# Kernel optimization log

Measured on AMD Instinct MI355X. Metric: run time of the kernel, lower is better.

Reference implementation:

```python
import jax, jax.numpy as jnp
import numpy as np

EPS = 1e-12  # matches torch F.normalize default eps in spectral_norm


def _l2norm(v):
    return v / jnp.maximum(jnp.linalg.norm(v), EPS)


def _spectral_norm(W, u):
    # One power-iteration step (torch spectral_norm training behavior).
    # u, v are treated as constants w.r.t. gradients.
    v = jax.lax.stop_gradient(_l2norm(W.T @ u))
    u2 = jax.lax.stop_gradient(_l2norm(W @ v))
    sigma = jnp.einsum('o,oi,i->', u2, W, v)
    return W / sigma


def setup_inputs() -> dict:
    key = jax.random.key(0)
    ks = jax.random.split(key, 8)
    B, C, N = 8, 512, 2048
    d = C // 8
    return {
        'x':  jax.random.normal(ks[0], (B, C, N), dtype=jnp.float32),
        'Wq': jax.random.normal(ks[1], (d, C), dtype=jnp.float32) * (1.0 / np.sqrt(C)),
        'Wk': jax.random.normal(ks[2], (d, C), dtype=jnp.float32) * (1.0 / np.sqrt(C)),
        'Wv': jax.random.normal(ks[3], (C, C), dtype=jnp.float32) * (1.0 / np.sqrt(C)),
        'uq': jax.random.normal(ks[4], (d,), dtype=jnp.float32),
        'uk': jax.random.normal(ks[5], (d,), dtype=jnp.float32),
        'uv': jax.random.normal(ks[6], (C,), dtype=jnp.float32),
        'gamma': jax.random.normal(ks[7], (1,), dtype=jnp.float32) * 0.1,
    }


def reference(x, Wq, Wk, Wv, uq, uk, uv, gamma):
    # x: [B, C, N]
    f = jnp.einsum('oi,bin->bon', _spectral_norm(Wq, uq), x)  # [B, C/8, N]
    g = jnp.einsum('oi,bin->bon', _spectral_norm(Wk, uk), x)  # [B, C/8, N]
    h = jnp.einsum('oi,bin->bon', _spectral_norm(Wv, uv), x)  # [B, C, N]
    scores = jnp.einsum('bdn,bdm->bnm', f, g)                 # f^T g: [B, N, N]
    beta = jax.nn.softmax(scores, axis=1)                      # softmax over dim=1
    o = gamma[0] * jnp.einsum('bcn,bnm->bcm', h, beta) + x    # [B, C, N]
    return o
```

## Files before the change

### kernel.cpp

```cpp
#include <hip/hip_runtime.h>
#include <hip/hip_bf16.h>
#include <math.h>

#define B_ 8
#define C_ 512
#define N_ 2048
#define D_ 64
#define O_ 640

typedef __bf16 bf16x8 __attribute__((ext_vector_type(8)));
typedef float f32x4 __attribute__((ext_vector_type(4)));
typedef unsigned short ushort8_t __attribute__((ext_vector_type(8)));
typedef unsigned short ushort4_t __attribute__((ext_vector_type(4)));

__device__ __forceinline__ unsigned short f2bf(float f) {
    unsigned int u = __builtin_bit_cast(unsigned int, f);
    u += 0x7fffu + ((u >> 16) & 1u);
    return (unsigned short)(u >> 16);
}

__device__ __forceinline__ unsigned short f2bf_hw(float f) {
    __bf16 h = (__bf16)f;
    return __builtin_bit_cast(unsigned short, h);
}

__device__ __forceinline__ float fastexp(float x) {
    return exp2f(x * 1.44269504088896340736f);
}

union FragU { ushort8_t u; bf16x8 b; };

__device__ __forceinline__ bf16x8 ldfrag(const unsigned short* p) {
    FragU t; t.u = *(const ushort8_t*)p; return t.b;
}

__device__ __forceinline__ void gload_lds16(const unsigned short* g, unsigned short* l) {
    __builtin_amdgcn_global_load_lds((const __attribute__((address_space(1))) void*)g,
                                     (__attribute__((address_space(3))) void*)l,
                                     16, 0, 0);
}

__global__ __launch_bounds__(512) void k_colvec(const float* __restrict__ Wq,
                                                const float* __restrict__ Wk,
                                                const float* __restrict__ Wv,
                                                const float* __restrict__ uq,
                                                const float* __restrict__ uk,
                                                const float* __restrict__ uv,
                                                float* __restrict__ tpart) {
    int which = blockIdx.y, oq = blockIdx.x;
    const float* W; const float* u; int R;
    if (which == 0)      { W = Wq; u = uq; R = 64;  }
    else if (which == 1) { W = Wk; u = uk; R = 64;  }
    else                 { W = Wv; u = uv; R = 512; }
    int chunk = R >> 2;
    int i = threadIdx.x;
    float s = 0.f;
    int o0 = oq * chunk, o1 = o0 + chunk;
    for (int o = o0; o < o1; ++o) s += W[(size_t)o * 512 + i] * u[o];
    tpart[((which << 2) + oq) * 512 + i] = s;
}

__global__ __launch_bounds__(512) void k_trow(const float* __restrict__ tpart,
                                              float* __restrict__ tvec,
                                              float* __restrict__ t2) {
    int which = blockIdx.x, i = threadIdx.x;
    const float* tp = tpart + (which << 2) * 512;
    float s = tp[i] + tp[512 + i] + tp[1024 + i] + tp[1536 + i];
    tvec[which * 512 + i] = s;
    __shared__ float red[512];
    red[i] = s * s; __syncthreads();
    for (int st = 256; st > 0; st >>= 1) { if (i < st) red[i] += red[i + st]; __syncthreads(); }
    if (i == 0) t2[which] = red[0];
}

__global__ __launch_bounds__(256) void k_rowvec(const float* __restrict__ Wq,
                                                const float* __restrict__ Wk,
                                                const float* __restrict__ Wv,
                                                const float* __restrict__ tvec,
                                                float* __restrict__ wpart) {
    int which = blockIdx.y;
    const float* W; int R;
    if (which == 0)      { W = Wq; R = 64;  }
    else if (which == 1) { W = Wk; R = 64;  }
    else                 { W = Wv; R = 512; }
    int tid = threadIdx.x, lane = tid & 63, wv = tid >> 6;
    int row = blockIdx.x * 4 + wv;
    float ps = 0.f;
    if (row < R) {
        const float4* wr_ = (const float4*)(W + (size_t)row * 512);
        const float4* tv = (const float4*)(tvec + which * 512);
        float4 a0 = wr_[lane * 2], a1 = wr_[lane * 2 + 1];
        float4 b0 = tv[lane * 2], b1 = tv[lane * 2 + 1];
        float s = a0.x * b0.x + a0.y * b0.y + a0.z * b0.z + a0.w * b0.w
                + a1.x * b1.x + a1.y * b1.y + a1.z * b1.z + a1.w * b1.w;
        #pragma unroll
        for (int off = 1; off < 64; off <<= 1) s += __shfl_xor(s, off, 64);
        ps = s * s;
    }
    __shared__ float red[4];
    if (lane == 0) red[wv] = ps;
    __syncthreads();
    if (tid == 0) wpart[which * 128 + blockIdx.x] = red[0] + red[1] + red[2] + red[3];
}

__global__ __launch_bounds__(128) void k_scale(const float* __restrict__ wpart,
                                               const float* __restrict__ t2,
                                               float* __restrict__ scales) {
    int which = blockIdx.x, tid = threadIdx.x;
    float s = wpart[which * 128 + tid];
    #pragma unroll
    for (int off = 1; off < 64; off <<= 1) s += __shfl_xor(s, off, 64);
    __shared__ float r2[2];
    if ((tid & 63) == 0) r2[tid >> 6] = s;
    __syncthreads();
    if (tid == 0) scales[which] = sqrtf(t2[which] / fmaxf(r2[0] + r2[1], 1e-24f));
}

__global__ __launch_bounds__(256) void k_wconv(const float* __restrict__ Wq,
                                               const float* __restrict__ Wk,
                                               const float* __restrict__ Wv,
                                               const float* __restrict__ scales,
                                               unsigned short* __restrict__ Wb) {
    int gid = blockIdx.x * 256 + threadIdx.x;
    int e0 = gid * 8;
    int o = e0 >> 9, i = e0 & 511;
    const float* src; float sc;
    if (o < 64)       { src = Wq + (size_t)o * 512;         sc = scales[0]; }
    else if (o < 128) { src = Wk + (size_t)(o - 64) * 512;  sc = scales[1]; }
    else              { src = Wv + (size_t)(o - 128) * 512; sc = scales[2]; }
    float4 v0 = *(const float4*)(src + i), v1 = *(const float4*)(src + i + 4);
    ushort8_t u;
    u[0] = f2bf(v0.x * sc); u[1] = f2bf(v0.y * sc); u[2] = f2bf(v0.z * sc); u[3] = f2bf(v0.w * sc);
    u[4] = f2bf(v1.x * sc); u[5] = f2bf(v1.y * sc); u[6] = f2bf(v1.z * sc); u[7] = f2bf(v1.w * sc);
    *(ushort8_t*)&Wb[(size_t)o * 512 + i] = u;
}

__global__ __launch_bounds__(256) void k_transpose(const float* __restrict__ x,
                                                   unsigned short* __restrict__ xT) {
    __shared__ float tile[64][33];
    int b = blockIdx.z;
    int n0 = blockIdx.x * 32, c0 = blockIdx.y * 64;
    int tx = threadIdx.x, ty = threadIdx.y;
    #pragma unroll
    for (int k = 0; k < 8; ++k) {
        int c = ty + k * 8;
        tile[c][tx] = x[((size_t)b * C_ + c0 + c) * N_ + n0 + tx];
    }
    __syncthreads();
    #pragma unroll
    for (int k = 0; k < 4; ++k) {
        int n = ty + k * 8;
        unsigned int p = (unsigned int)f2bf(tile[tx * 2][n]) |
                         ((unsigned int)f2bf(tile[tx * 2 + 1][n]) << 16);
        *(unsigned int*)&xT[((size_t)b * N_ + n0 + n) * C_ + c0 + tx * 2] = p;
    }
}

__global__ __launch_bounds__(256) void k_proj(const unsigned short* __restrict__ xT,
                                              const unsigned short* __restrict__ Wb,
                                              unsigned short* __restrict__ fT,
                                              unsigned short* __restrict__ gT,
                                              unsigned short* __restrict__ hb) {
    int b = blockIdx.z, n0 = blockIdx.y * 128, o0 = blockIdx.x * 128;
    int tid = threadIdx.x, lane = tid & 63, w = tid >> 6;
    int wr = w >> 1, wc = w & 1;
    __shared__ __align__(16) unsigned short Sh[16384];
    unsigned short* As = Sh;
    unsigned short* Bs = Sh + 8192;
    f32x4 zero = {0.f, 0.f, 0.f, 0.f};
    f32x4 acc[4][4];
    #pragma unroll
    for (int i = 0; i < 4; ++i)
        #pragma unroll
        for (int j = 0; j < 4; ++j) acc[i][j] = zero;
    int r8 = lane >> 3, s = lane & 7;
    int scol = (s ^ r8) * 8;

    for (int kt = 0; kt < 8; ++kt) {
        #pragma unroll
        for (int q = 0; q < 4; ++q) {
            int chunk = w * 4 + q;
            int row = chunk * 8 + r8;
            gload_lds16(xT + ((size_t)b * N_ + n0 + row) * C_ + kt * 64 + scol, &As[chunk * 512]);
            gload_lds16(Wb + (size_t)(o0 + row) * C_ + kt * 64 + scol, &Bs[chunk * 512]);
        }
        __syncthreads();
        int kg = lane >> 4, r16 = lane & 15;
        #pragma unroll
        for (int kk = 0; kk < 2; ++kk) {
            int sw = kk * 4 + kg;
            bf16x8 af[4];
            #pragma unroll
            for (int i = 0; i < 4; ++i) {
                int row = wr * 64 + i * 16 + r16;
                af[i] = ldfrag(&As[row * 64 + (sw ^ (row & 7)) * 8]);
            }
            #pragma unroll
            for (int j = 0; j < 4; ++j) {
                int row = wc * 64 + j * 16 + r16;
                bf16x8 bv = ldfrag(&Bs[row * 64 + (sw ^ (row & 7)) * 8]);
                #pragma unroll
                for (int i = 0; i < 4; ++i)
                    acc[i][j] = __builtin_amdgcn_mfma_f32_16x16x32_bf16(af[i], bv, acc[i][j], 0, 0, 0);
            }
        }
        __syncthreads();
    }

    unsigned short* St = Sh;
    if (o0 == 0) {
        #pragma unroll
        for (int p = 0; p < 2; ++p) {
            if (wc == p) {
                #pragma unroll
                for (int i = 0; i < 4; ++i)
                    #pragma unroll
                    for (int j = 0; j < 4; ++j)
                        #pragma unroll
                        for (int r = 0; r < 4; ++r)
                            St[(wr * 64 + i * 16 + (lane >> 4) * 4 + r) * 72 + j * 16 + (lane & 15)] = f2bf(acc[i][j][r]);
            }
            __syncthreads();
            unsigned short* dst = p == 0 ? fT : gT;
            #pragma unroll
            for (int it = 0; it < 4; ++it) {
                int row = it * 32 + (tid >> 3);
                *(ushort8_t*)&dst[((size_t)b * N_ + n0 + row) * D_ + (tid & 7) * 8] =
                    *(ushort8_t*)&St[row * 72 + (tid & 7) * 8];
            }
            __syncthreads();
        }
    } else {
        int ho0 = o0 - 128;
        #pragma unroll
        for (int p = 0; p < 2; ++p) {
            if (wc == p) {
                #pragma unroll
                for (int i = 0; i < 4; ++i)
                    #pragma unroll
                    for (int j = 0; j < 4; ++j)
                        #pragma unroll
                        for (int r = 0; r < 4; ++r)
                            St[(j * 16 + (lane & 15)) * 136 + wr * 64 + i * 16 + (lane >> 4) * 4 + r] = f2bf(acc[i][j][r]);
            }
            __syncthreads();
            #pragma unroll
            for (int it = 0; it < 4; ++it) {
                int row = it * 16 + (tid >> 4);
                *(ushort8_t*)&hb[((size_t)b * C_ + ho0 + p * 64 + row) * N_ + n0 + (tid & 15) * 8] =
                    *(ushort8_t*)&St[row * 136 + (tid & 15) * 8];
            }
            __syncthreads();
        }
    }
}

__global__ __launch_bounds__(256) void k_stats(const unsigned short* __restrict__ fT,
                                               const unsigned short* __restrict__ gT,
                                               float* __restrict__ colmax,
                                               float* __restrict__ colsinv) {
    int b = blockIdx.y, m0 = blockIdx.x * 16;
    int tid = threadIdx.x, lane = tid & 63, w = tid >> 6;
    int mcol = m0 + (lane & 15);
    const unsigned short* gbase = gT + ((size_t)b * N_ + mcol) * D_ + (lane >> 4) * 8;
    bf16x8 g0 = ldfrag(gbase);
    bf16x8 g1 = ldfrag(gbase + 32);

    float mx = -1e30f, sm = 0.f;
    for (int nt = w * 32; nt < w * 32 + 32; ++nt) {
        const unsigned short* abase = fT + ((size_t)b * N_ + nt * 16 + (lane & 15)) * D_ + (lane >> 4) * 8;
        f32x4 s = {0.f, 0.f, 0.f, 0.f};
        s = __builtin_amdgcn_mfma_f32_16x16x32_bf16(ldfrag(abase), g0, s, 0, 0, 0);
        s = __builtin_amdgcn_mfma_f32_16x16x32_bf16(ldfrag(abase + 32), g1, s, 0, 0, 0);
        float tm = fmaxf(fmaxf(s[0], s[1]), fmaxf(s[2], s[3]));
        float nm = fmaxf(mx, tm);
        float c = fastexp(mx - nm);
        sm = sm * c + fastexp(s[0] - nm) + fastexp(s[1] - nm) + fastexp(s[2] - nm) + fastexp(s[3] - nm);
        mx = nm;
    }
    #pragma unroll
    for (int off = 16; off < 64; off <<= 1) {
        float omx = __shfl_xor(mx, off, 64);
        float osm = __shfl_xor(sm, off, 64);
        float nm = fmaxf(mx, omx);
        sm = sm * fastexp(mx - nm) + osm * fastexp(omx - nm);
        mx = nm;
    }
    __shared__ float lmx[4][16], lsm[4][16];
    if ((lane >> 4) == 0) { lmx[w][lane & 15] = mx; lsm[w][lane & 15] = sm; }
    __syncthreads();
    if (tid < 16) {
        float M = lmx[0][tid], S = lsm[0][tid];
        #pragma unroll
        for (int q = 1; q < 4; ++q) {
            float om = lmx[q][tid], os = lsm[q][tid];
            float nm = fmaxf(M, om);
            S = S * fastexp(M - nm) + os * fastexp(om - nm);
            M = nm;
        }
        colmax[(size_t)b * N_ + m0 + tid] = M;
        colsinv[(size_t)b * N_ + m0 + tid] = 1.0f / S;
    }
}

__global__ __launch_bounds__(512, 4) void k_av(const unsigned short* __restrict__ fT,
                                               const unsigned short* __restrict__ gT,
                                               const unsigned short* __restrict__ hb,
                                               const float* __restrict__ colmax,
                                               const float* __restrict__ colsinv,
                                               const float* __restrict__ x,
                                               const float* __restrict__ gamma,
                                               float* __restrict__ out) {
    __shared__ __align__(16) unsigned short FT[2][4096];
    __shared__ __align__(16) unsigned short HB[16384];
    __shared__ __align__(16) unsigned short BS[2][4096];

    const int NT = N_ / 64;
    int bid = blockIdx.x;
    int xg = bid & 7, sidx = bid >> 3;
    int mi = sidx & 31, gh = sidx >> 5;
    int g = xg + 8 * gh;
    int b = g >> 1, ch = g & 1;
    int m0 = mi * 64, c0 = ch * 256;

    int tid = threadIdx.x, lane = tid & 63, w = tid >> 6;
    int nw = w & 3, mh = w >> 2;
    int l15 = lane & 15, lq = lane >> 4;
    int r8 = lane >> 3, sl = lane & 7;
    int scol = (sl ^ r8) * 8;

    const float LOG2E = 1.44269504088896340736f;
    bf16x8 gf[2][2];
    float off_[2];
    #pragma unroll
    for (int j = 0; j < 2; ++j) {
        int m = m0 + mh * 32 + j * 16 + l15;
        #pragma unroll
        for (int kd = 0; kd < 2; ++kd)
            gf[j][kd] = ldfrag(gT + ((size_t)b * N_ + m) * D_ + kd * 32 + lq * 8);
        off_[j] = log2f(colsinv[(size_t)b * N_ + m]) - colmax[(size_t)b * N_ + m] * LOG2E;
    }

    f32x4 zero = {0.f, 0.f, 0.f, 0.f};
    f32x4 acc[2][4];
    #pragma unroll
    for (int i = 0; i < 2; ++i)
        #pragma unroll
        for (int j = 0; j < 4; ++j) acc[i][j] = zero;

    const unsigned short* fbase = fT + ((size_t)b * N_) * D_;
    const unsigned short* hbase = hb + ((size_t)b * C_ + c0) * N_;

    ushort8_t hreg0, hreg1, hreg2, hreg3;

    auto HLOAD = [&](int kt) {
        const unsigned short* p0 = hbase + (size_t)((w * 4 + 0) * 8 + r8) * N_ + kt * 64 + scol;
        const unsigned short* p1 = hbase + (size_t)((w * 4 + 1) * 8 + r8) * N_ + kt * 64 + scol;
        const unsigned short* p2 = hbase + (size_t)((w * 4 + 2) * 8 + r8) * N_ + kt * 64 + scol;
        const unsigned short* p3 = hbase + (size_t)((w * 4 + 3) * 8 + r8) * N_ + kt * 64 + scol;
        hreg0 = *(const ushort8_t*)p0;
        hreg1 = *(const ushort8_t*)p1;
        hreg2 = *(const ushort8_t*)p2;
        hreg3 = *(const ushort8_t*)p3;
    };
    auto HWRITE = [&]() {
        *(ushort8_t*)&HB[(w * 4 + 0) * 512 + lane * 8] = hreg0;
        *(ushort8_t*)&HB[(w * 4 + 1) * 512 + lane * 8] = hreg1;
        *(ushort8_t*)&HB[(w * 4 + 2) * 512 + lane * 8] = hreg2;
        *(ushort8_t*)&HB[(w * 4 + 3) * 512 + lane * 8] = hreg3;
    };
    auto STAGE_FT = [&](int kt, int p) {
        gload_lds16(fbase + ((size_t)kt * 64 + w * 8 + r8) * D_ + scol, &FT[p][w * 512]);
    };
    auto SPHASE = [&](int p) {
        int arow = nw * 16 + l15;
        bf16x8 af0 = ldfrag(&FT[p][arow * 64 + ((lq ^ (arow & 7)) * 8)]);
        bf16x8 af1 = ldfrag(&FT[p][arow * 64 + (((4 + lq) ^ (arow & 7)) * 8)]);
        #pragma unroll
        for (int j = 0; j < 2; ++j) {
            f32x4 sv = zero;
            sv = __builtin_amdgcn_mfma_f32_16x16x32_bf16(af0, gf[j][0], sv, 0, 0, 0);
            sv = __builtin_amdgcn_mfma_f32_16x16x32_bf16(af1, gf[j][1], sv, 0, 0, 0);
            int mrel = mh * 32 + j * 16 + l15;
            ushort4_t pk;
            #pragma unroll
            for (int r = 0; r < 4; ++r)
                pk[r] = f2bf_hw(exp2f(fmaf(sv[r], LOG2E, off_[j])));
            int nt = nw * 16 + lq * 4;
            *(ushort4_t*)&BS[p][mrel * 64 + (((nt >> 3) ^ (mrel & 7)) * 8) + (nt & 7)] = pk;
        }
    };
    auto PVPHASE = [&](int p) {
        __builtin_amdgcn_s_setprio(1);
        #pragma unroll
        for (int kk = 0; kk < 2; ++kk) {
            int ng = kk * 4 + lq;
            bf16x8 pa[2];
            #pragma unroll
            for (int i = 0; i < 2; ++i) {
                int mr = mh * 32 + i * 16 + l15;
                pa[i] = ldfrag(&BS[p][mr * 64 + ((ng ^ (mr & 7)) * 8)]);
            }
            #pragma unroll
            for (int j = 0; j < 4; ++j) {
                int cr = nw * 64 + j * 16 + l15;
                bf16x8 hv = ldfrag(&HB[cr * 64 + ((ng ^ (cr & 7)) * 8)]);
                #pragma unroll
                for (int i = 0; i < 2; ++i)
                    acc[i][j] = __builtin_amdgcn_mfma_f32_16x16x32_bf16(pa[i], hv, acc[i][j], 0, 0, 0);
            }
        }
        __builtin_amdgcn_s_setprio(0);
    };

    STAGE_FT(0, 0);
    HLOAD(0);
    asm volatile("s_waitcnt vmcnt(0)" ::: "memory");
    __builtin_amdgcn_sched_barrier(0);
    HWRITE();
    asm volatile("s_waitcnt lgkmcnt(0)" ::: "memory");
    __builtin_amdgcn_sched_barrier(0);
    __builtin_amdgcn_s_barrier();
    __builtin_amdgcn_sched_barrier(0);
    SPHASE(0);
    asm volatile("s_waitcnt lgkmcnt(0)" ::: "memory");
    __builtin_amdgcn_sched_barrier(0);
    __builtin_amdgcn_s_barrier();
    __builtin_amdgcn_sched_barrier(0);

    #pragma unroll 1
    for (int kt = 0; kt < NT; ++kt) {
        int p = kt & 1;
        if (kt + 1 < NT) {
            HLOAD(kt + 1);
            STAGE_FT(kt + 1, p ^ 1);
            __builtin_amdgcn_sched_barrier(0);
        }
        PVPHASE(p);
        if (kt + 1 < NT) {
            asm volatile("s_waitcnt vmcnt(0)" ::: "memory");
            __builtin_amdgcn_sched_barrier(0);
            __builtin_amdgcn_s_barrier();
            __builtin_amdgcn_sched_barrier(0);
            HWRITE();
            SPHASE(p ^ 1);
            asm volatile("s_waitcnt lgkmcnt(0)" ::: "memory");
            __builtin_amdgcn_sched_barrier(0);
            __builtin_amdgcn_s_barrier();
            __builtin_amdgcn_sched_barrier(0);
        }
    }

    float gv = gamma[0];
    #pragma unroll
    for (int i = 0; i < 2; ++i) {
        int mabs = m0 + mh * 32 + i * 16 + lq * 4;
        #pragma unroll
        for (int j = 0; j < 4; ++j) {
            int cabs = c0 + nw * 64 + j * 16 + l15;
            size_t base = ((size_t)b * C_ + cabs) * N_ + mabs;
            float4 xv = *(const float4*)(x + base);
            float4 ov;
            ov.x = gv * acc[i][j][0] + xv.x;
            ov.y = gv * acc[i][j][1] + xv.y;
            ov.z = gv * acc[i][j][2] + xv.z;
            ov.w = gv * acc[i][j][3] + xv.w;
            *(float4*)(out + base) = ov;
        }
    }
}

extern "C" void kernel_launch(void* const* d_in, const int* in_sizes, int n_in,
                              void* d_out, int out_size, void* d_ws, size_t ws_size,
                              hipStream_t stream) {
    const float* x     = (const float*)d_in[0];
    const float* Wq    = (const float*)d_in[1];
    const float* Wk    = (const float*)d_in[2];
    const float* Wv    = (const float*)d_in[3];
    const float* uq    = (const float*)d_in[4];
    const float* uk    = (const float*)d_in[5];
    const float* uv    = (const float*)d_in[6];
    const float* gamma = (const float*)d_in[7];
    float* out = (float*)d_out;

    char* wsb = (char*)d_ws;
    float* scales         = (float*)wsb;
    unsigned short* xT    = (unsigned short*)(wsb + 256);
    unsigned short* fT    = xT + (size_t)B_ * N_ * C_;
    unsigned short* gT    = fT + (size_t)B_ * N_ * D_;
    unsigned short* hb    = gT + (size_t)B_ * N_ * D_;
    float* colmax         = (float*)(hb + (size_t)B_ * C_ * N_);
    float* colsinv        = colmax + (size_t)B_ * N_;
    float* tpart          = colsinv + (size_t)B_ * N_;
    float* tvec           = tpart + 3 * 4 * 512;
    float* t2             = tvec + 3 * 512;
    float* wpart          = t2 + 16;
    unsigned short* Wb    = (unsigned short*)(wpart + 3 * 128);

    k_colvec<<<dim3(4, 3), 512, 0, stream>>>(Wq, Wk, Wv, uq, uk, uv, tpart);
    k_trow<<<3, 512, 0, stream>>>(tpart, tvec, t2);
    k_rowvec<<<dim3(128, 3), 256, 0, stream>>>(Wq, Wk, Wv, tvec, wpart);
    k_scale<<<3, 128, 0, stream>>>(wpart, t2, scales);
    k_wconv<<<O_ * C_ / (256 * 8), 256, 0, stream>>>(Wq, Wk, Wv, scales, Wb);
    k_transpose<<<dim3(N_ / 32, C_ / 64, B_), dim3(32, 8), 0, stream>>>(x, xT);
    k_proj<<<dim3(O_ / 128, N_ / 128, B_), 256, 0, stream>>>(xT, Wb, fT, gT, hb);
    k_stats<<<dim3(N_ / 16, B_), 256, 0, stream>>>(fT, gT, colmax, colsinv);
    k_av<<<512, 512, 0, stream>>>(fT, gT, hb, colmax, colsinv, x, gamma, out);
}
```

Before: 173.5 us.

## Load f fragments directly to registers in k_av and remap grids for XCD locality

```diff
diff --git a/kernel.cpp b/kernel.cpp
--- a/kernel.cpp
+++ b/kernel.cpp
@@ -32,6 +32,10 @@
 
 __device__ __forceinline__ bf16x8 ldfrag(const unsigned short* p) {
     FragU t; t.u = *(const ushort8_t*)p; return t.b;
+}
+
+__device__ __forceinline__ bf16x8 asfrag(ushort8_t u) {
+    FragU t; t.u = u; return t.b;
 }
 
 __device__ __forceinline__ void gload_lds16(const unsigned short* g, unsigned short* l) {
@@ -161,7 +165,13 @@
                                               unsigned short* __restrict__ fT,
                                               unsigned short* __restrict__ gT,
                                               unsigned short* __restrict__ hb) {
-    int b = blockIdx.z, n0 = blockIdx.y * 128, o0 = blockIdx.x * 128;
+    int bid = blockIdx.x;
+    int xcd = bid & 7, r = bid >> 3;
+    int o_t = r % 5;
+    int sub = (r / 5) & 1;
+    int b = r / 10;
+    int n0 = (xcd * 2 + sub) * 128, o0 = o_t * 128;
+
     int tid = threadIdx.x, lane = tid & 63, w = tid >> 6;
     int wr = w >> 1, wc = w & 1;
     __shared__ __align__(16) unsigned short Sh[16384];
@@ -173,8 +183,8 @@
     for (int i = 0; i < 4; ++i)
         #pragma unroll
         for (int j = 0; j < 4; ++j) acc[i][j] = zero;
-    int r8 = lane >> 3, s = lane & 7;
-    int scol = (s ^ r8) * 8;
+    int r8 = lane >> 3, sl = lane & 7;
+    int scol = (sl ^ r8) * 8;
 
     for (int kt = 0; kt < 8; ++kt) {
         #pragma unroll
@@ -217,8 +227,8 @@
                     #pragma unroll
                     for (int j = 0; j < 4; ++j)
                         #pragma unroll
-                        for (int r = 0; r < 4; ++r)
-                            St[(wr * 64 + i * 16 + (lane >> 4) * 4 + r) * 72 + j * 16 + (lane & 15)] = f2bf(acc[i][j][r]);
+                        for (int r2_ = 0; r2_ < 4; ++r2_)
+                            St[(wr * 64 + i * 16 + (lane >> 4) * 4 + r2_) * 72 + j * 16 + (lane & 15)] = f2bf(acc[i][j][r2_]);
             }
             __syncthreads();
             unsigned short* dst = p == 0 ? fT : gT;
@@ -240,8 +250,8 @@
                     #pragma unroll
                     for (int j = 0; j < 4; ++j)
                         #pragma unroll
-                        for (int r = 0; r < 4; ++r)
-                            St[(j * 16 + (lane & 15)) * 136 + wr * 64 + i * 16 + (lane >> 4) * 4 + r] = f2bf(acc[i][j][r]);
+                        for (int r2_ = 0; r2_ < 4; ++r2_)
+                            St[(j * 16 + (lane & 15)) * 136 + wr * 64 + i * 16 + (lane >> 4) * 4 + r2_] = f2bf(acc[i][j][r2_]);
             }
             __syncthreads();
             #pragma unroll
@@ -259,7 +269,8 @@
                                                const unsigned short* __restrict__ gT,
                                                float* __restrict__ colmax,
                                                float* __restrict__ colsinv) {
-    int b = blockIdx.y, m0 = blockIdx.x * 16;
+    int bid = blockIdx.x;
+    int b = bid & 7, m0 = (bid >> 3) * 16;
     int tid = threadIdx.x, lane = tid & 63, w = tid >> 6;
     int mcol = m0 + (lane & 15);
     const unsigned short* gbase = gT + ((size_t)b * N_ + mcol) * D_ + (lane >> 4) * 8;
@@ -311,7 +322,6 @@
                                                const float* __restrict__ x,
                                                const float* __restrict__ gamma,
                                                float* __restrict__ out) {
-    __shared__ __align__(16) unsigned short FT[2][4096];
     __shared__ __align__(16) unsigned short HB[16384];
     __shared__ __align__(16) unsigned short BS[2][4096];
 
@@ -352,16 +362,13 @@
     const unsigned short* hbase = hb + ((size_t)b * C_ + c0) * N_;
 
     ushort8_t hreg0, hreg1, hreg2, hreg3;
+    ushort8_t freg0, freg1;
 
     auto HLOAD = [&](int kt) {
-        const unsigned short* p0 = hbase + (size_t)((w * 4 + 0) * 8 + r8) * N_ + kt * 64 + scol;
-        const unsigned short* p1 = hbase + (size_t)((w * 4 + 1) * 8 + r8) * N_ + kt * 64 + scol;
-        const unsigned short* p2 = hbase + (size_t)((w * 4 + 2) * 8 + r8) * N_ + kt * 64 + scol;
-        const unsigned short* p3 = hbase + (size_t)((w * 4 + 3) * 8 + r8) * N_ + kt * 64 + scol;
-        hreg0 = *(const ushort8_t*)p0;
-        hreg1 = *(const ushort8_t*)p1;
-        hreg2 = *(const ushort8_t*)p2;
-        hreg3 = *(const ushort8_t*)p3;
+        hreg0 = *(const ushort8_t*)(hbase + (size_t)((w * 4 + 0) * 8 + r8) * N_ + kt * 64 + scol);
+        hreg1 = *(const ushort8_t*)(hbase + (size_t)((w * 4 + 1) * 8 + r8) * N_ + kt * 64 + scol);
+        hreg2 = *(const ushort8_t*)(hbase + (size_t)((w * 4 + 2) * 8 + r8) * N_ + kt * 64 + scol);
+        hreg3 = *(const ushort8_t*)(hbase + (size_t)((w * 4 + 3) * 8 + r8) * N_ + kt * 64 + scol);
     };
     auto HWRITE = [&]() {
         *(ushort8_t*)&HB[(w * 4 + 0) * 512 + lane * 8] = hreg0;
@@ -369,13 +376,14 @@
         *(ushort8_t*)&HB[(w * 4 + 2) * 512 + lane * 8] = hreg2;
         *(ushort8_t*)&HB[(w * 4 + 3) * 512 + lane * 8] = hreg3;
     };
-    auto STAGE_FT = [&](int kt, int p) {
-        gload_lds16(fbase + ((size_t)kt * 64 + w * 8 + r8) * D_ + scol, &FT[p][w * 512]);
+    auto FLOAD = [&](int kt) {
+        const unsigned short* fp = fbase + ((size_t)kt * 64 + nw * 16 + l15) * D_ + lq * 8;
+        freg0 = *(const ushort8_t*)fp;
+        freg1 = *(const ushort8_t*)(fp + 32);
     };
     auto SPHASE = [&](int p) {
-        int arow = nw * 16 + l15;
-        bf16x8 af0 = ldfrag(&FT[p][arow * 64 + ((lq ^ (arow & 7)) * 8)]);
-        bf16x8 af1 = ldfrag(&FT[p][arow * 64 + (((4 + lq) ^ (arow & 7)) * 8)]);
+        bf16x8 af0 = asfrag(freg0);
+        bf16x8 af1 = asfrag(freg1);
         #pragma unroll
         for (int j = 0; j < 2; ++j) {
             f32x4 sv = zero;
@@ -413,15 +421,11 @@
         __builtin_amdgcn_s_setprio(0);
     };
 
-    STAGE_FT(0, 0);
     HLOAD(0);
+    FLOAD(0);
     asm volatile("s_waitcnt vmcnt(0)" ::: "memory");
     __builtin_amdgcn_sched_barrier(0);
     HWRITE();
-    asm volatile("s_waitcnt lgkmcnt(0)" ::: "memory");
-    __builtin_amdgcn_sched_barrier(0);
-    __builtin_amdgcn_s_barrier();
-    __builtin_amdgcn_sched_barrier(0);
     SPHASE(0);
     asm volatile("s_waitcnt lgkmcnt(0)" ::: "memory");
     __builtin_amdgcn_sched_barrier(0);
@@ -433,7 +437,7 @@
         int p = kt & 1;
         if (kt + 1 < NT) {
             HLOAD(kt + 1);
-            STAGE_FT(kt + 1, p ^ 1);
+            FLOAD(kt + 1);
             __builtin_amdgcn_sched_barrier(0);
         }
         PVPHASE(p);
@@ -503,7 +507,7 @@
     k_scale<<<3, 128, 0, stream>>>(wpart, t2, scales);
     k_wconv<<<O_ * C_ / (256 * 8), 256, 0, stream>>>(Wq, Wk, Wv, scales, Wb);
     k_transpose<<<dim3(N_ / 32, C_ / 64, B_), dim3(32, 8), 0, stream>>>(x, xT);
-    k_proj<<<dim3(O_ / 128, N_ / 128, B_), 256, 0, stream>>>(xT, Wb, fT, gT, hb);
-    k_stats<<<dim3(N_ / 16, B_), 256, 0, stream>>>(fT, gT, colmax, colsinv);
+    k_proj<<<640, 256, 0, stream>>>(xT, Wb, fT, gT, hb);
+    k_stats<<<1024, 256, 0, stream>>>(fT, gT, colmax, colsinv);
     k_av<<<512, 512, 0, stream>>>(fT, gT, hb, colmax, colsinv, x, gamma, out);
 }
```

After: 174.9 us. No clear change (+0.8%).
